# Kernel tuning notes

Measured on AMD Instinct MI355X. Metric: run time of the kernel, lower is better.

The kernel has to match this reference:

```python
import jax, jax.numpy as jnp
import numpy as np

K = 4  # Chebyshev order (init kwarg k)


def _spmm(rows, cols, vals, x, n_nodes):
    # sparse [N,N] @ dense [N,D] via gather + segment_sum
    return jax.ops.segment_sum(vals[:, None] * x[cols], rows, num_segments=n_nodes)


def setup_inputs() -> dict:
    key = jax.random.key(0)
    k_x, k_r, k_c, k_v, k_w = jax.random.split(key, 5)
    N, E, D_IN, D_OUT = 50000, 800000, 128, 128
    inp = {
        "input": jax.random.normal(k_x, (N, D_IN), dtype=jnp.float32),
        "adj_rows": jax.random.randint(k_r, (E,), 0, N, dtype=jnp.int32),
        "adj_cols": jax.random.randint(k_c, (E,), 0, N, dtype=jnp.int32),
        "adj_vals": jax.random.uniform(k_v, (E,), dtype=jnp.float32) * 0.1,
        # xavier_uniform for W [in_dim, out_dim]
        "W": jax.random.uniform(k_w, (D_IN, D_OUT), dtype=jnp.float32,
                                 minval=-1.0, maxval=1.0) * np.sqrt(6.0 / (D_IN + D_OUT)),
    }
    return inp


def reference(input, adj_rows, adj_cols, adj_vals, W):
    n = input.shape[0]
    xs = []
    for i in range(K):
        if i == 0:
            xs.append(input @ W)
        elif i == 1:
            # faithful to original: support computed but unused; xs[1] == xs[0]
            xs.append(input @ W)
        else:
            support = _spmm(adj_rows, adj_cols, 2.0 * adj_vals, xs[i - 1], n) - xs[i - 2]
            xs.append(support @ W)
    return xs[-1]
```

## Files before the change

### kernel.cpp

```cpp
#include <hip/hip_runtime.h>
#include <cstddef>
#include <cstdint>

#define THREADS 256
#define KPART 256
#define MAXNB 1600

typedef short bf16x8 __attribute__((ext_vector_type(8)));
typedef float f32x4 __attribute__((ext_vector_type(4)));
typedef unsigned short u16x8 __attribute__((ext_vector_type(8)));

#define GLOBAL_AS __attribute__((address_space(1)))
#define LDS_AS    __attribute__((address_space(3)))

__device__ __forceinline__ void async_copy16(const void* g, void* l) {
    __builtin_amdgcn_global_load_lds((const GLOBAL_AS void*)g, (LDS_AS void*)l, 16, 0, 0);
}

__device__ __forceinline__ ushort f2bf(float f) {
    uint32_t u = __float_as_uint(f);
    u = u + 0x7FFFu + ((u >> 16) & 1u);
    return (ushort)(u >> 16);
}
__device__ __forceinline__ float bf2f(ushort h) {
    return __uint_as_float(((uint32_t)h) << 16);
}

__device__ __forceinline__ void rowfma(float4& acc, const float4 xv,
                                       const float4 w0, const float4 w1,
                                       const float4 w2, const float4 w3) {
    acc.x = fmaf(xv.x, w0.x, acc.x); acc.y = fmaf(xv.x, w0.y, acc.y);
    acc.z = fmaf(xv.x, w0.z, acc.z); acc.w = fmaf(xv.x, w0.w, acc.w);
    acc.x = fmaf(xv.y, w1.x, acc.x); acc.y = fmaf(xv.y, w1.y, acc.y);
    acc.z = fmaf(xv.y, w1.z, acc.z); acc.w = fmaf(xv.y, w1.w, acc.w);
    acc.x = fmaf(xv.z, w2.x, acc.x); acc.y = fmaf(xv.z, w2.y, acc.y);
    acc.z = fmaf(xv.z, w2.z, acc.z); acc.w = fmaf(xv.z, w2.w, acc.w);
    acc.x = fmaf(xv.w, w3.x, acc.x); acc.y = fmaf(xv.w, w3.y, acc.y);
    acc.z = fmaf(xv.w, w3.z, acc.z); acc.w = fmaf(xv.w, w3.w, acc.w);
}

__device__ __forceinline__ void mm32(const float4* Ws4, const float4* Xs4,
                                     int c4, int rb,
                                     float4& a0, float4& a1, float4& a2, float4& a3) {
#pragma unroll 4
    for (int kq = 0; kq < 32; ++kq) {
        float4 w0 = Ws4[(4 * kq + 0) * 32 + c4];
        float4 w1 = Ws4[(4 * kq + 1) * 32 + c4];
        float4 w2 = Ws4[(4 * kq + 2) * 32 + c4];
        float4 w3 = Ws4[(4 * kq + 3) * 32 + c4];
        float4 x0 = Xs4[(rb + 0) * 32 + kq];
        float4 x1 = Xs4[(rb + 1) * 32 + kq];
        float4 x2 = Xs4[(rb + 2) * 32 + kq];
        float4 x3 = Xs4[(rb + 3) * 32 + kq];
        rowfma(a0, x0, w0, w1, w2, w3);
        rowfma(a1, x1, w0, w1, w2, w3);
        rowfma(a2, x2, w0, w1, w2, w3);
        rowfma(a3, x3, w0, w1, w2, w3);
    }
}

__global__ __launch_bounds__(256, 2)
void wpow_kernel(const float* __restrict__ W,
                 ushort* __restrict__ w3t_hi, ushort* __restrict__ w3t_lo,
                 ushort* __restrict__ nw2t_hi, ushort* __restrict__ nw2t_lo) {
    __shared__ float4 Ws4[128 * 32];
    __shared__ float4 Xs4[32 * 32];
    const int tid = threadIdx.x;
    const int row0 = (blockIdx.x & 3) * 32;
    const bool is3 = blockIdx.x >= 4;
    const float4* __restrict__ W4 = (const float4*)W;

#pragma unroll
    for (int i = 0; i < 16; ++i) Ws4[tid + i * 256] = W4[tid + i * 256];
#pragma unroll
    for (int i = 0; i < 4; ++i) {
        int li = tid + i * 256;
        Xs4[li] = W4[(size_t)(row0 + (li >> 5)) * 32 + (li & 31)];
    }
    __syncthreads();

    const int c4 = tid & 31;
    const int rb = (tid >> 5) * 4;
    float4 a0 = {0.f, 0.f, 0.f, 0.f};
    float4 a1 = {0.f, 0.f, 0.f, 0.f};
    float4 a2 = {0.f, 0.f, 0.f, 0.f};
    float4 a3 = {0.f, 0.f, 0.f, 0.f};
    mm32(Ws4, Xs4, c4, rb, a0, a1, a2, a3);

    if (is3) {
        __syncthreads();
        Xs4[(rb + 0) * 32 + c4] = a0;
        Xs4[(rb + 1) * 32 + c4] = a1;
        Xs4[(rb + 2) * 32 + c4] = a2;
        Xs4[(rb + 3) * 32 + c4] = a3;
        __syncthreads();
        a0 = {0.f, 0.f, 0.f, 0.f};
        a1 = {0.f, 0.f, 0.f, 0.f};
        a2 = {0.f, 0.f, 0.f, 0.f};
        a3 = {0.f, 0.f, 0.f, 0.f};
        mm32(Ws4, Xs4, c4, rb, a0, a1, a2, a3);
    }

    ushort* __restrict__ dh = is3 ? w3t_hi : nw2t_hi;
    ushort* __restrict__ dl = is3 ? w3t_lo : nw2t_lo;
    const float sgn = is3 ? 1.0f : -1.0f;
    const int r = row0 + rb;
#pragma unroll
    for (int i = 0; i < 4; ++i) {
        float4 a = (i == 0) ? a0 : (i == 1) ? a1 : (i == 2) ? a2 : a3;
        const int k = r + i;
#pragma unroll
        for (int e = 0; e < 4; ++e) {
            float v = ((e == 0) ? a.x : (e == 1) ? a.y : (e == 2) ? a.z : a.w) * sgn;
            int c = c4 * 4 + e;
            int idx = c * 128 + (k ^ ((c & 7) << 3));
            ushort h = f2bf(v);
            dh[idx] = h;
            dl[idx] = f2bf(v - bf2f(h));
        }
    }
}

__global__ __launch_bounds__(256, 2)
void gemm_dual_mfma(const float* __restrict__ A1, const ushort* __restrict__ B1h,
                    const ushort* __restrict__ B1l,
                    const float* __restrict__ A2, const ushort* __restrict__ B2h,
                    const ushort* __restrict__ B2l,
                    float* __restrict__ out, int N) {
    __shared__ ushort WtHi[16384];
    __shared__ ushort WtLo[16384];
    __shared__ ushort XsHi[4096];
    __shared__ ushort XsLo[4096];
    const int tid = threadIdx.x;
    const int row0 = blockIdx.x * 32;
    const int l = tid & 63, w = tid >> 6;
    const int mt = w & 1, ntb = (w >> 1) * 4;
    const int fr = l & 15, fh = l >> 4;

    f32x4 acc[4];
#pragma unroll
    for (int nt = 0; nt < 4; ++nt) acc[nt] = (f32x4){0.f, 0.f, 0.f, 0.f};

    for (int pass = 0; pass < 2; ++pass) {
        const float* __restrict__ Asrc = pass ? A2 : A1;
        const ushort* __restrict__ Bh = pass ? B2h : B1h;
        const ushort* __restrict__ Bl = pass ? B2l : B1l;
        if (pass) __syncthreads();

#pragma unroll
        for (int i = 0; i < 8; ++i) {
            async_copy16(Bh + tid * 8 + i * 2048, WtHi + tid * 8 + i * 2048);
            async_copy16(Bl + tid * 8 + i * 2048, WtLo + tid * 8 + i * 2048);
        }

        {
            const int row = tid >> 3, kb = (tid & 7) * 16;
            int gr = row0 + row;
            if (gr >= N) gr = N - 1;
            const float4* __restrict__ ap =
                (const float4*)(Asrc + (size_t)gr * 128) + (kb >> 2);
            float4 v0 = ap[0], v1 = ap[1], v2 = ap[2], v3 = ap[3];
            float f[16] = {v0.x, v0.y, v0.z, v0.w, v1.x, v1.y, v1.z, v1.w,
                           v2.x, v2.y, v2.z, v2.w, v3.x, v3.y, v3.z, v3.w};
            ushort hi[16], lo[16];
#pragma unroll
            for (int i = 0; i < 16; ++i) {
                hi[i] = f2bf(f[i]);
                lo[i] = f2bf(f[i] - bf2f(hi[i]));
            }
#pragma unroll
            for (int g = 0; g < 2; ++g) {
                int idx = row * 128 + ((kb + 8 * g) ^ ((row & 7) << 3));
                bf16x8 vh, vl;
#pragma unroll
                for (int j = 0; j < 8; ++j) {
                    vh[j] = (short)hi[8 * g + j];
                    vl[j] = (short)lo[8 * g + j];
                }
                *(bf16x8*)&XsHi[idx] = vh;
                *(bf16x8*)&XsLo[idx] = vl;
            }
        }
        __syncthreads();

#pragma unroll
        for (int ks = 0; ks < 4; ++ks) {
            const int arow = mt * 16 + fr;
            const int aoff = arow * 128 + ((ks * 32 + fh * 8) ^ ((arow & 7) << 3));
            bf16x8 ah = *(const bf16x8*)&XsHi[aoff];
            bf16x8 al = *(const bf16x8*)&XsLo[aoff];
#pragma unroll
            for (int nt = 0; nt < 4; ++nt) {
                const int brow = (ntb + nt) * 16 + fr;
                const int boff = brow * 128 + ((ks * 32 + fh * 8) ^ ((brow & 7) << 3));
                bf16x8 bh = *(const bf16x8*)&WtHi[boff];
                bf16x8 bl = *(const bf16x8*)&WtLo[boff];
                acc[nt] = __builtin_amdgcn_mfma_f32_16x16x32_bf16(ah, bh, acc[nt], 0, 0, 0);
                acc[nt] = __builtin_amdgcn_mfma_f32_16x16x32_bf16(al, bh, acc[nt], 0, 0, 0);
                acc[nt] = __builtin_amdgcn_mfma_f32_16x16x32_bf16(ah, bl, acc[nt], 0, 0, 0);
            }
        }
    }

#pragma unroll
    for (int nt = 0; nt < 4; ++nt) {
        const int col = (ntb + nt) * 16 + fr;
#pragma unroll
        for (int i = 0; i < 4; ++i) {
            const int rr = row0 + mt * 16 + fh * 4 + i;
            if (rr < N) out[(size_t)rr * 128 + col] = acc[nt][i];
        }
    }
}


__global__ void part_count_conv_kernel(const int* __restrict__ erows, int E,
                                       int* __restrict__ blockcounts, int NB, int chunk,
                                       const float* __restrict__ X,
                                       ushort* __restrict__ Xbf, int ngroups, int cb) {
    __shared__ int hist[MAXNB];
    const int b = blockIdx.x;
    const int tid = threadIdx.x;
    if (b < cb) {
        int i = b * 256 + tid;
        if (i < ngroups) {
            const float4* __restrict__ X4 = (const float4*)X;
            float4 v0 = X4[i * 2 + 0];
            float4 v1 = X4[i * 2 + 1];
            u16x8 o;
            o[0] = f2bf(v0.x); o[1] = f2bf(v0.y); o[2] = f2bf(v0.z); o[3] = f2bf(v0.w);
            o[4] = f2bf(v1.x); o[5] = f2bf(v1.y); o[6] = f2bf(v1.z); o[7] = f2bf(v1.w);
            ((u16x8*)Xbf)[i] = o;
        }
        return;
    }
    const int k = b - cb;
    for (int i = tid; i < NB; i += 256) hist[i] = 0;
    __syncthreads();
    const int e0 = k * chunk;
    const int e1 = (e0 + chunk < E) ? e0 + chunk : E;
    for (int i = e0 + tid; i < e1; i += 256)
        atomicAdd(&hist[erows[i] >> 5], 1);
    __syncthreads();
    for (int i = tid; i < NB; i += 256) blockcounts[i * KPART + k] = hist[i];
}

__global__ void part_scan1_kernel(int* __restrict__ blockcounts,
                                  int* __restrict__ btotal, int NB) {
    const int tid = threadIdx.x;
    const int lane = tid & 63;
    const int b = blockIdx.x * 4 + (tid >> 6);
    if (b >= NB) return;
    int* __restrict__ row = blockcounts + (size_t)b * KPART;
    int c0 = row[lane * 4 + 0];
    int c1 = row[lane * 4 + 1];
    int c2 = row[lane * 4 + 2];
    int c3 = row[lane * 4 + 3];
    int lsum = c0 + c1 + c2 + c3;
    int s = lsum;
#pragma unroll
    for (int off = 1; off < 64; off <<= 1) {
        int t = __shfl_up(s, off);
        if (lane >= off) s += t;
    }
    int run = s - lsum;
    row[lane * 4 + 0] = run; run += c0;
    row[lane * 4 + 1] = run; run += c1;
    row[lane * 4 + 2] = run; run += c2;
    row[lane * 4 + 3] = run;
    if (lane == 63) btotal[b] = s;
}

__global__ __launch_bounds__(1024)
void part_scan2_kernel(const int* __restrict__ btotal, int* __restrict__ bbase,
                       int NB, int E, int* __restrict__ rowptr, int N) {
    __shared__ int sums[1024];
    const int tid = threadIdx.x;
    const int items = (NB + 1023) >> 10;
    const int start = tid * items;
    const int end = (start + items < NB) ? start + items : NB;
    int s = 0;
    for (int i = start; i < end; ++i) s += btotal[i];
    sums[tid] = s;
    __syncthreads();
#pragma unroll
    for (int off = 1; off < 1024; off <<= 1) {
        int t = (tid >= off) ? sums[tid - off] : 0;
        __syncthreads();
        sums[tid] += t;
        __syncthreads();
    }
    int run = sums[tid] - s;
    for (int i = start; i < end; ++i) {
        bbase[i] = run;
        run += btotal[i];
    }
    if (tid == 0) { bbase[NB] = E; rowptr[N] = E; }
}

__global__ void part_place_kernel(const int* __restrict__ erows,
                                  const int* __restrict__ ecols,
                                  const float* __restrict__ evals, int E,
                                  const int* __restrict__ blockcounts,
                                  const int* __restrict__ bbase, int NB, int chunk,
                                  int2* __restrict__ bucketed) {
    __shared__ int cur[MAXNB];
    const int k = blockIdx.x;
    const int tid = threadIdx.x;
    for (int i = tid; i < NB; i += 256)
        cur[i] = bbase[i] + blockcounts[(size_t)i * KPART + k];
    __syncthreads();
    const int e0 = k * chunk;
    const int e1 = (e0 + chunk < E) ? e0 + chunk : E;
    for (int i = e0 + tid; i < e1; i += 256) {
        int r = erows[i];
        int pos = atomicAdd(&cur[r >> 5], 1);
        int2 p;
        p.x = (int)(((uint32_t)(r & 31) << 16) | (uint32_t)ecols[i]);
        p.y = __float_as_int(2.0f * evals[i]);
        bucketed[pos] = p;
    }
}

__global__ void part_finish_kernel(const int2* __restrict__ bucketed,
                                   const int* __restrict__ bbase,
                                   int* __restrict__ rowptr,
                                   int2* __restrict__ csr, int N) {
    __shared__ int rcnt[32];
    __shared__ int rpos[32];
    const int b = blockIdx.x;
    const int tid = threadIdx.x;
    const int base = bbase[b];
    const int end = bbase[b + 1];
    const int row0 = b * 32;
    if (tid < 32) rcnt[tid] = 0;
    __syncthreads();
    for (int i = base + tid; i < end; i += 256)
        atomicAdd(&rcnt[((uint32_t)bucketed[i].x) >> 16], 1);
    __syncthreads();
    if (tid == 0) {
        int run = base;
        for (int j = 0; j < 32; ++j) {
            int c = rcnt[j];
            rpos[j] = run;
            if (row0 + j < N) rowptr[row0 + j] = run;
            run += c;
        }
    }
    __syncthreads();
    for (int i = base + tid; i < end; i += 256) {
        int2 e = bucketed[i];
        uint32_t meta = (uint32_t)e.x;
        int pos = atomicAdd(&rpos[meta >> 16], 1);
        int2 p;
        p.x = (int)(meta & 0xFFFFu);
        p.y = e.y;
        csr[pos] = p;
    }
}

__device__ __forceinline__ float4 bf4f(ushort4 v) {
    float4 r;
    r.x = bf2f(v.x); r.y = bf2f(v.y); r.z = bf2f(v.z); r.w = bf2f(v.w);
    return r;
}

template <bool WRITE_BF>
__global__ __launch_bounds__(256, 8)
void spmm_gather_bf(const int* __restrict__ rowptr, const int2* __restrict__ csr,
                    const ushort* __restrict__ src, const float* __restrict__ init,
                    void* __restrict__ dst, int N) {
    long long idx = (long long)blockIdx.x * blockDim.x + threadIdx.x;
    int row = (int)(idx >> 5);
    if (row >= N) return;
    int lane = (int)(idx & 31);
    const ushort4* __restrict__ S4 = (const ushort4*)src;
    float4 accA = {0.f, 0.f, 0.f, 0.f};
    float4 accB = {0.f, 0.f, 0.f, 0.f};
    if (init) {
        float4 t = ((const float4*)init)[(size_t)row * 32 + lane];
        accA.x = -t.x; accA.y = -t.y; accA.z = -t.z; accA.w = -t.w;
    }
    int p = rowptr[row];
    const int p1 = rowptr[row + 1];
    for (; p + 7 < p1; p += 8) {
        int2 cv0 = csr[p + 0];
        int2 cv1 = csr[p + 1];
        int2 cv2 = csr[p + 2];
        int2 cv3 = csr[p + 3];
        int2 cv4 = csr[p + 4];
        int2 cv5 = csr[p + 5];
        int2 cv6 = csr[p + 6];
        int2 cv7 = csr[p + 7];
        float4 x0 = bf4f(S4[(size_t)cv0.x * 32 + lane]);
        float4 x1 = bf4f(S4[(size_t)cv1.x * 32 + lane]);
        float4 x2 = bf4f(S4[(size_t)cv2.x * 32 + lane]);
        float4 x3 = bf4f(S4[(size_t)cv3.x * 32 + lane]);
        float4 x4 = bf4f(S4[(size_t)cv4.x * 32 + lane]);
        float4 x5 = bf4f(S4[(size_t)cv5.x * 32 + lane]);
        float4 x6 = bf4f(S4[(size_t)cv6.x * 32 + lane]);
        float4 x7 = bf4f(S4[(size_t)cv7.x * 32 + lane]);
        float v0 = __int_as_float(cv0.y);
        float v1 = __int_as_float(cv1.y);
        float v2 = __int_as_float(cv2.y);
        float v3 = __int_as_float(cv3.y);
        float v4 = __int_as_float(cv4.y);
        float v5 = __int_as_float(cv5.y);
        float v6 = __int_as_float(cv6.y);
        float v7 = __int_as_float(cv7.y);
        accA.x = fmaf(v0, x0.x, accA.x); accA.y = fmaf(v0, x0.y, accA.y);
        accA.z = fmaf(v0, x0.z, accA.z); accA.w = fmaf(v0, x0.w, accA.w);
        accB.x = fmaf(v1, x1.x, accB.x); accB.y = fmaf(v1, x1.y, accB.y);
        accB.z = fmaf(v1, x1.z, accB.z); accB.w = fmaf(v1, x1.w, accB.w);
        accA.x = fmaf(v2, x2.x, accA.x); accA.y = fmaf(v2, x2.y, accA.y);
        accA.z = fmaf(v2, x2.z, accA.z); accA.w = fmaf(v2, x2.w, accA.w);
        accB.x = fmaf(v3, x3.x, accB.x); accB.y = fmaf(v3, x3.y, accB.y);
        accB.z = fmaf(v3, x3.z, accB.z); accB.w = fmaf(v3, x3.w, accB.w);
        accA.x = fmaf(v4, x4.x, accA.x); accA.y = fmaf(v4, x4.y, accA.y);
        accA.z = fmaf(v4, x4.z, accA.z); accA.w = fmaf(v4, x4.w, accA.w);
        accB.x = fmaf(v5, x5.x, accB.x); accB.y = fmaf(v5, x5.y, accB.y);
        accB.z = fmaf(v5, x5.z, accB.z); accB.w = fmaf(v5, x5.w, accB.w);
        accA.x = fmaf(v6, x6.x, accA.x); accA.y = fmaf(v6, x6.y, accA.y);
        accA.z = fmaf(v6, x6.z, accA.z); accA.w = fmaf(v6, x6.w, accA.w);
        accB.x = fmaf(v7, x7.x, accB.x); accB.y = fmaf(v7, x7.y, accB.y);
        accB.z = fmaf(v7, x7.z, accB.z); accB.w = fmaf(v7, x7.w, accB.w);
    }
    for (; p + 3 < p1; p += 4) {
        int2 cv0 = csr[p + 0];
        int2 cv1 = csr[p + 1];
        int2 cv2 = csr[p + 2];
        int2 cv3 = csr[p + 3];
        float4 x0 = bf4f(S4[(size_t)cv0.x * 32 + lane]);
        float4 x1 = bf4f(S4[(size_t)cv1.x * 32 + lane]);
        float4 x2 = bf4f(S4[(size_t)cv2.x * 32 + lane]);
        float4 x3 = bf4f(S4[(size_t)cv3.x * 32 + lane]);
        float v0 = __int_as_float(cv0.y);
        float v1 = __int_as_float(cv1.y);
        float v2 = __int_as_float(cv2.y);
        float v3 = __int_as_float(cv3.y);
        accA.x = fmaf(v0, x0.x, accA.x); accA.y = fmaf(v0, x0.y, accA.y);
        accA.z = fmaf(v0, x0.z, accA.z); accA.w = fmaf(v0, x0.w, accA.w);
        accB.x = fmaf(v1, x1.x, accB.x); accB.y = fmaf(v1, x1.y, accB.y);
        accB.z = fmaf(v1, x1.z, accB.z); accB.w = fmaf(v1, x1.w, accB.w);
        accA.x = fmaf(v2, x2.x, accA.x); accA.y = fmaf(v2, x2.y, accA.y);
        accA.z = fmaf(v2, x2.z, accA.z); accA.w = fmaf(v2, x2.w, accA.w);
        accB.x = fmaf(v3, x3.x, accB.x); accB.y = fmaf(v3, x3.y, accB.y);
        accB.z = fmaf(v3, x3.z, accB.z); accB.w = fmaf(v3, x3.w, accB.w);
    }
    for (; p < p1; ++p) {
        int2 cv = csr[p];
        float v = __int_as_float(cv.y);
        float4 x = bf4f(S4[(size_t)cv.x * 32 + lane]);
        accA.x = fmaf(v, x.x, accA.x);
        accA.y = fmaf(v, x.y, accA.y);
        accA.z = fmaf(v, x.z, accA.z);
        accA.w = fmaf(v, x.w, accA.w);
    }
    float4 acc;
    acc.x = accA.x + accB.x;
    acc.y = accA.y + accB.y;
    acc.z = accA.z + accB.z;
    acc.w = accA.w + accB.w;
    if (WRITE_BF) {
        ushort4 o;
        o.x = f2bf(acc.x); o.y = f2bf(acc.y); o.z = f2bf(acc.z); o.w = f2bf(acc.w);
        ((ushort4*)dst)[(size_t)row * 32 + lane] = o;
    } else {
        ((float4*)dst)[(size_t)row * 32 + lane] = acc;
    }
}

extern "C" void kernel_launch(void* const* d_in, const int* in_sizes, int n_in,
                              void* d_out, int out_size, void* d_ws, size_t ws_size,
                              hipStream_t stream) {
    const float* X     = (const float*)d_in[0];
    const int*   erows = (const int*)d_in[1];
    const int*   ecols = (const int*)d_in[2];
    const float* evals = (const float*)d_in[3];
    const float* W     = (const float*)d_in[4];
    float* out = (float*)d_out;

    const int N = in_sizes[0] / 128;
    const int E = in_sizes[1];

    ushort* t2bf    = (ushort*)d_ws;
    float*  u2      = (float*)(t2bf + (size_t)N * 128);
    int2*   bucketed= (int2*)u2;
    ushort* xbf     = (ushort*)(u2 + (size_t)N * 128);
    ushort* wtab    = xbf + (size_t)N * 128;
    ushort* w3t_hi  = wtab;
    ushort* w3t_lo  = wtab + 16384;
    ushort* nw2t_hi = wtab + 32768;
    ushort* nw2t_lo = wtab + 49152;
    int2*   csr     = (int2*)(wtab + 65536);
    int*    rowptr  = (int*)(csr + E);
    int*    blkcnt  = rowptr + (N + 1);
    const int NB    = (N + 31) >> 5;
    int*    btotal  = blkcnt + (size_t)NB * KPART;
    int*    bbase   = btotal + NB;

    const int chunk    = (E + KPART - 1) / KPART;
    const int ngroups  = N * 16;
    const int cb       = (ngroups + 255) / 256;
    const int g_blocks = (int)(((long long)N * 32 + 255) / 256);
    const int d_blocks = (N + 31) / 32;

    wpow_kernel<<<8, THREADS, 0, stream>>>(W, w3t_hi, w3t_lo, nw2t_hi, nw2t_lo);

    part_count_conv_kernel<<<cb + KPART, THREADS, 0, stream>>>(erows, E, blkcnt, NB,
                                                               chunk, X, xbf, ngroups, cb);
    part_scan1_kernel<<<(NB + 3) / 4, THREADS, 0, stream>>>(blkcnt, btotal, NB);
    part_scan2_kernel<<<1, 1024, 0, stream>>>(btotal, bbase, NB, E, rowptr, N);
    part_place_kernel<<<KPART, THREADS, 0, stream>>>(erows, ecols, evals, E, blkcnt,
                                                     bbase, NB, chunk, bucketed);
    part_finish_kernel<<<NB, THREADS, 0, stream>>>(bucketed, bbase, rowptr, csr, N);

    spmm_gather_bf<true><<<g_blocks, THREADS, 0, stream>>>(rowptr, csr, xbf, X, t2bf, N);
    spmm_gather_bf<false><<<g_blocks, THREADS, 0, stream>>>(rowptr, csr, t2bf, nullptr, u2, N);
    gemm_dual_mfma<<<d_blocks, THREADS, 0, stream>>>(u2, w3t_hi, w3t_lo,
                                                     X, nw2t_hi, nw2t_lo, out, N);
}
```

Before: 150.6 us.

## Fuse second SpMM gather into dual MFMA GEMM, reading weights from global

Merges the second sparse gather with the final dual-pass MFMA GEMM, so each block gathers its 32 rows of A·T2 straight into LDS as hi/lo bf16 and skips the fp32 u2 round trip through global memory. The weight tiles are now read directly from global/L2 instead of being staged in LDS. This cuts LDS use so launch bounds can allow 4 blocks per SM. The gather phase now runs with only 32 rows per block, 4 rows per wave-half, which may lower memory-level parallelism. The bucketed scratch buffer is moved so it no longer aliases u2.

```diff
diff --git a/kernel.cpp b/kernel.cpp
--- a/kernel.cpp
+++ b/kernel.cpp
@@ -9,13 +9,6 @@
 typedef short bf16x8 __attribute__((ext_vector_type(8)));
 typedef float f32x4 __attribute__((ext_vector_type(4)));
 typedef unsigned short u16x8 __attribute__((ext_vector_type(8)));
-
-#define GLOBAL_AS __attribute__((address_space(1)))
-#define LDS_AS    __attribute__((address_space(3)))
-
-__device__ __forceinline__ void async_copy16(const void* g, void* l) {
-    __builtin_amdgcn_global_load_lds((const GLOBAL_AS void*)g, (LDS_AS void*)l, 16, 0, 0);
-}
 
 __device__ __forceinline__ ushort f2bf(float f) {
     uint32_t u = __float_as_uint(f);
@@ -121,99 +114,6 @@
     }
 }
 
-__global__ __launch_bounds__(256, 2)
-void gemm_dual_mfma(const float* __restrict__ A1, const ushort* __restrict__ B1h,
-                    const ushort* __restrict__ B1l,
-                    const float* __restrict__ A2, const ushort* __restrict__ B2h,
-                    const ushort* __restrict__ B2l,
-                    float* __restrict__ out, int N) {
-    __shared__ ushort WtHi[16384];
-    __shared__ ushort WtLo[16384];
-    __shared__ ushort XsHi[4096];
-    __shared__ ushort XsLo[4096];
-    const int tid = threadIdx.x;
-    const int row0 = blockIdx.x * 32;
-    const int l = tid & 63, w = tid >> 6;
-    const int mt = w & 1, ntb = (w >> 1) * 4;
-    const int fr = l & 15, fh = l >> 4;
-
-    f32x4 acc[4];
-#pragma unroll
-    for (int nt = 0; nt < 4; ++nt) acc[nt] = (f32x4){0.f, 0.f, 0.f, 0.f};
-
-    for (int pass = 0; pass < 2; ++pass) {
-        const float* __restrict__ Asrc = pass ? A2 : A1;
-        const ushort* __restrict__ Bh = pass ? B2h : B1h;
-        const ushort* __restrict__ Bl = pass ? B2l : B1l;
-        if (pass) __syncthreads();
-
-#pragma unroll
-        for (int i = 0; i < 8; ++i) {
-            async_copy16(Bh + tid * 8 + i * 2048, WtHi + tid * 8 + i * 2048);
-            async_copy16(Bl + tid * 8 + i * 2048, WtLo + tid * 8 + i * 2048);
-        }
-
-        {
-            const int row = tid >> 3, kb = (tid & 7) * 16;
-            int gr = row0 + row;
-            if (gr >= N) gr = N - 1;
-            const float4* __restrict__ ap =
-                (const float4*)(Asrc + (size_t)gr * 128) + (kb >> 2);
-            float4 v0 = ap[0], v1 = ap[1], v2 = ap[2], v3 = ap[3];
-            float f[16] = {v0.x, v0.y, v0.z, v0.w, v1.x, v1.y, v1.z, v1.w,
-                           v2.x, v2.y, v2.z, v2.w, v3.x, v3.y, v3.z, v3.w};
-            ushort hi[16], lo[16];
-#pragma unroll
-            for (int i = 0; i < 16; ++i) {
-                hi[i] = f2bf(f[i]);
-                lo[i] = f2bf(f[i] - bf2f(hi[i]));
-            }
-#pragma unroll
-            for (int g = 0; g < 2; ++g) {
-                int idx = row * 128 + ((kb + 8 * g) ^ ((row & 7) << 3));
-                bf16x8 vh, vl;
-#pragma unroll
-                for (int j = 0; j < 8; ++j) {
-                    vh[j] = (short)hi[8 * g + j];
-                    vl[j] = (short)lo[8 * g + j];
-                }
-                *(bf16x8*)&XsHi[idx] = vh;
-                *(bf16x8*)&XsLo[idx] = vl;
-            }
-        }
-        __syncthreads();
-
-#pragma unroll
-        for (int ks = 0; ks < 4; ++ks) {
-            const int arow = mt * 16 + fr;
-            const int aoff = arow * 128 + ((ks * 32 + fh * 8) ^ ((arow & 7) << 3));
-            bf16x8 ah = *(const bf16x8*)&XsHi[aoff];
-            bf16x8 al = *(const bf16x8*)&XsLo[aoff];
-#pragma unroll
-            for (int nt = 0; nt < 4; ++nt) {
-                const int brow = (ntb + nt) * 16 + fr;
-                const int boff = brow * 128 + ((ks * 32 + fh * 8) ^ ((brow & 7) << 3));
-                bf16x8 bh = *(const bf16x8*)&WtHi[boff];
-                bf16x8 bl = *(const bf16x8*)&WtLo[boff];
-                acc[nt] = __builtin_amdgcn_mfma_f32_16x16x32_bf16(ah, bh, acc[nt], 0, 0, 0);
-                acc[nt] = __builtin_amdgcn_mfma_f32_16x16x32_bf16(al, bh, acc[nt], 0, 0, 0);
-                acc[nt] = __builtin_amdgcn_mfma_f32_16x16x32_bf16(ah, bl, acc[nt], 0, 0, 0);
-            }
-        }
-    }
-
-#pragma unroll
-    for (int nt = 0; nt < 4; ++nt) {
-        const int col = (ntb + nt) * 16 + fr;
-#pragma unroll
-        for (int i = 0; i < 4; ++i) {
-            const int rr = row0 + mt * 16 + fh * 4 + i;
-            if (rr < N) out[(size_t)rr * 128 + col] = acc[nt][i];
-        }
-    }
-}
-
-
 __global__ void part_count_conv_kernel(const int* __restrict__ erows, int E,
                                        int* __restrict__ blockcounts, int NB, int chunk,
                                        const float* __restrict__ X,
@@ -365,22 +265,12 @@
     return r;
 }
 
-template <bool WRITE_BF>
-__global__ __launch_bounds__(256, 8)
-void spmm_gather_bf(const int* __restrict__ rowptr, const int2* __restrict__ csr,
-                    const ushort* __restrict__ src, const float* __restrict__ init,
-                    void* __restrict__ dst, int N) {
-    long long idx = (long long)blockIdx.x * blockDim.x + threadIdx.x;
-    int row = (int)(idx >> 5);
-    if (row >= N) return;
-    int lane = (int)(idx & 31);
-    const ushort4* __restrict__ S4 = (const ushort4*)src;
+__device__ __forceinline__ float4 gather_row_bf16(const int* __restrict__ rowptr,
+                                                  const int2* __restrict__ csr,
+                                                  const ushort4* __restrict__ S4,
+                                                  int row, int lane) {
     float4 accA = {0.f, 0.f, 0.f, 0.f};
     float4 accB = {0.f, 0.f, 0.f, 0.f};
-    if (init) {
-        float4 t = ((const float4*)init)[(size_t)row * 32 + lane];
-        accA.x = -t.x; accA.y = -t.y; accA.z = -t.z; accA.w = -t.w;
-    }
     int p = rowptr[row];
     const int p1 = rowptr[row + 1];
     for (; p + 7 < p1; p += 8) {
@@ -461,12 +351,138 @@
     acc.y = accA.y + accB.y;
     acc.z = accA.z + accB.z;
     acc.w = accA.w + accB.w;
-    if (WRITE_BF) {
-        ushort4 o;
-        o.x = f2bf(acc.x); o.y = f2bf(acc.y); o.z = f2bf(acc.z); o.w = f2bf(acc.w);
-        ((ushort4*)dst)[(size_t)row * 32 + lane] = o;
-    } else {
-        ((float4*)dst)[(size_t)row * 32 + lane] = acc;
+    return acc;
+}
+
+__global__ __launch_bounds__(256, 8)
+void spmm1_kernel(const int* __restrict__ rowptr, const int2* __restrict__ csr,
+                  const ushort* __restrict__ src, const float* __restrict__ init,
+                  ushort* __restrict__ dst, int N) {
+    long long idx = (long long)blockIdx.x * blockDim.x + threadIdx.x;
+    int row = (int)(idx >> 5);
+    if (row >= N) return;
+    int lane = (int)(idx & 31);
+    float4 acc = gather_row_bf16(rowptr, csr, (const ushort4*)src, row, lane);
+    float4 t = ((const float4*)init)[(size_t)row * 32 + lane];
+    acc.x -= t.x; acc.y -= t.y; acc.z -= t.z; acc.w -= t.w;
+    ushort4 o;
+    o.x = f2bf(acc.x); o.y = f2bf(acc.y); o.z = f2bf(acc.z); o.w = f2bf(acc.w);
+    ((ushort4*)dst)[(size_t)row * 32 + lane] = o;
+}
+
+__global__ __launch_bounds__(256, 4)
+void spmm_gemm_fused(const int* __restrict__ rowptr, const int2* __restrict__ csr,
+                     const ushort* __restrict__ t2bf, const float* __restrict__ X,
+                     const ushort* __restrict__ B1h, const ushort* __restrict__ B1l,
+                     const ushort* __restrict__ B2h, const ushort* __restrict__ B2l,
+                     float* __restrict__ out, int N) {
+    __shared__ ushort XsHi[4096];
+    __shared__ ushort XsLo[4096];
+    const int tid = threadIdx.x;
+    const int row0 = blockIdx.x * 32;
+    const int l = tid & 63, w = tid >> 6;
+    const int mt = w & 1, ntb = (w >> 1) * 4;
+    const int fr = l & 15, fh = l >> 4;
+
+    f32x4 acc[4];
+#pragma unroll
+    for (int nt = 0; nt < 4; ++nt) acc[nt] = (f32x4){0.f, 0.f, 0.f, 0.f};
+
+    {
+        const int lane = tid & 31;
+        const ushort4* __restrict__ T4 = (const ushort4*)t2bf;
+#pragma unroll
+        for (int it = 0; it < 4; ++it) {
+            const int rl = (tid >> 5) * 4 + it;
+            const int row = row0 + rl;
+            float4 u = {0.f, 0.f, 0.f, 0.f};
+            if (row < N) u = gather_row_bf16(rowptr, csr, T4, row, lane);
+            ushort4 hv, lv;
+            hv.x = f2bf(u.x); lv.x = f2bf(u.x - bf2f(hv.x));
+            hv.y = f2bf(u.y); lv.y = f2bf(u.y - bf2f(hv.y));
+            hv.z = f2bf(u.z); lv.z = f2bf(u.z - bf2f(hv.z));
+            hv.w = f2bf(u.w); lv.w = f2bf(u.w - bf2f(hv.w));
+            const int idx = rl * 128 + ((4 * lane) ^ ((rl & 7) << 3));
+            *(ushort4*)&XsHi[idx] = hv;
+            *(ushort4*)&XsLo[idx] = lv;
+        }
+    }
+    __syncthreads();
+
+#pragma unroll
+    for (int ks = 0; ks < 4; ++ks) {
+        const int arow = mt * 16 + fr;
+        const int aoff = arow * 128 + ((ks * 32 + fh * 8) ^ ((arow & 7) << 3));
+        bf16x8 ah = *(const bf16x8*)&XsHi[aoff];
+        bf16x8 al = *(const bf16x8*)&XsLo[aoff];
+#pragma unroll
+        for (int nt = 0; nt < 4; ++nt) {
+            const int brow = (ntb + nt) * 16 + fr;
+            const int boff = brow * 128 + ((ks * 32 + fh * 8) ^ ((brow & 7) << 3));
+            bf16x8 bh = *(const bf16x8*)&B1h[boff];
+            bf16x8 bl = *(const bf16x8*)&B1l[boff];
+            acc[nt] = __builtin_amdgcn_mfma_f32_16x16x32_bf16(ah, bh, acc[nt], 0, 0, 0);
+            acc[nt] = __builtin_amdgcn_mfma_f32_16x16x32_bf16(al, bh, acc[nt], 0, 0, 0);
+            acc[nt] = __builtin_amdgcn_mfma_f32_16x16x32_bf16(ah, bl, acc[nt], 0, 0, 0);
+        }
+    }
+    __syncthreads();
+
+    {
+        const int row = tid >> 3, kb = (tid & 7) * 16;
+        int gr = row0 + row;
+        if (gr >= N) gr = N - 1;
+        const float4* __restrict__ ap = (const float4*)(X + (size_t)gr * 128) + (kb >> 2);
+        float4 v0 = ap[0], v1 = ap[1], v2 = ap[2], v3 = ap[3];
+        float f[16] = {v0.x, v0.y, v0.z, v0.w, v1.x, v1.y, v1.z, v1.w,
+                       v2.x, v2.y, v2.z, v2.w, v3.x, v3.y, v3.z, v3.w};
+        ushort hi[16], lo[16];
+#pragma unroll
+        for (int i = 0; i < 16; ++i) {
+            hi[i] = f2bf(f[i]);
+            lo[i] = f2bf(f[i] - bf2f(hi[i]));
+        }
+#pragma unroll
+        for (int g = 0; g < 2; ++g) {
+            int idx = row * 128 + ((kb + 8 * g) ^ ((row & 7) << 3));
+            bf16x8 vh, vl;
+#pragma unroll
+            for (int j = 0; j < 8; ++j) {
+                vh[j] = (short)hi[8 * g + j];
+                vl[j] = (short)lo[8 * g + j];
+            }
+            *(bf16x8*)&XsHi[idx] = vh;
+            *(bf16x8*)&XsLo[idx] = vl;
+        }
+    }
+    __syncthreads();
+
+#pragma unroll
+    for (int ks = 0; ks < 4; ++ks) {
+        const int arow = mt * 16 + fr;
+        const int aoff = arow * 128 + ((ks * 32 + fh * 8) ^ ((arow & 7) << 3));
+        bf16x8 ah = *(const bf16x8*)&XsHi[aoff];
+        bf16x8 al = *(const bf16x8*)&XsLo[aoff];
+#pragma unroll
+        for (int nt = 0; nt < 4; ++nt) {
+            const int brow = (ntb + nt) * 16 + fr;
+            const int boff = brow * 128 + ((ks * 32 + fh * 8) ^ ((brow & 7) << 3));
+            bf16x8 bh = *(const bf16x8*)&B2h[boff];
+            bf16x8 bl = *(const bf16x8*)&B2l[boff];
+            acc[nt] = __builtin_amdgcn_mfma_f32_16x16x32_bf16(ah, bh, acc[nt], 0, 0, 0);
+            acc[nt] = __builtin_amdgcn_mfma_f32_16x16x32_bf16(al, bh, acc[nt], 0, 0, 0);
+            acc[nt] = __builtin_amdgcn_mfma_f32_16x16x32_bf16(ah, bl, acc[nt], 0, 0, 0);
+        }
+    }
+
+#pragma unroll
+    for (int nt = 0; nt < 4; ++nt) {
+        const int col = (ntb + nt) * 16 + fr;
+#pragma unroll
+        for (int i = 0; i < 4; ++i) {
+            const int rr = row0 + mt * 16 + fh * 4 + i;
+            if (rr < N) out[(size_t)rr * 128 + col] = acc[nt][i];
+        }
     }
 }
 
@@ -484,16 +500,15 @@
     const int E = in_sizes[1];
 
     ushort* t2bf    = (ushort*)d_ws;
-    float*  u2      = (float*)(t2bf + (size_t)N * 128);
-    int2*   bucketed= (int2*)u2;
-    ushort* xbf     = (ushort*)(u2 + (size_t)N * 128);
+    ushort* xbf     = t2bf + (size_t)N * 128;
     ushort* wtab    = xbf + (size_t)N * 128;
     ushort* w3t_hi  = wtab;
     ushort* w3t_lo  = wtab + 16384;
     ushort* nw2t_hi = wtab + 32768;
     ushort* nw2t_lo = wtab + 49152;
     int2*   csr     = (int2*)(wtab + 65536);
-    int*    rowptr  = (int*)(csr + E);
+    int2*   bucketed= csr + E;
+    int*    rowptr  = (int*)(bucketed + E);
     int*    blkcnt  = rowptr + (N + 1);
     const int NB    = (N + 31) >> 5;
     int*    btotal  = blkcnt + (size_t)NB * KPART;
@@ -515,8 +530,8 @@
                                                      bbase, NB, chunk, bucketed);
     part_finish_kernel<<<NB, THREADS, 0, stream>>>(bucketed, bbase, rowptr, csr, N);
 
-    spmm_gather_bf<true><<<g_blocks, THREADS, 0, stream>>>(rowptr, csr, xbf, X, t2bf, N);
-    spmm_gather_bf<false><<<g_blocks, THREADS, 0, stream>>>(rowptr, csr, t2bf, nullptr, u2, N);
-    gemm_dual_mfma<<<d_blocks, THREADS, 0, stream>>>(u2, w3t_hi, w3t_lo,
-                                                     X, nw2t_hi, nw2t_lo, out, N);
-}
+    spmm1_kernel<<<g_blocks, THREADS, 0, stream>>>(rowptr, csr, xbf, X, t2bf, N);
+    spmm_gemm_fused<<<d_blocks, THREADS, 0, stream>>>(rowptr, csr, t2bf, X,
+                                                      w3t_hi, w3t_lo, nw2t_hi, nw2t_lo,
+                                                      out, N);
+}
```

Measured after the change: 156.7 us. +4.1%, slower.
